# Optimization experiments

Measured on AMD Instinct MI355X. Metric: run time of the kernel, lower is better.

Reference implementation:

```python
import jax, jax.numpy as jnp
import numpy as np

N_NODES = 8192
IN_DIM = 512
H_DIM = 128


def setup_inputs() -> dict:
    key = jax.random.key(0)
    k1, k2, k3, k4 = jax.random.split(key, 4)
    h = jax.random.normal(k1, (N_NODES, IN_DIM), dtype=jnp.float32)
    adj = jax.random.randint(k2, (N_NODES, N_NODES), 0, 2).astype(jnp.float32)
    # xavier-uniform-style scales
    w_scale = float(np.sqrt(6.0 / (IN_DIM + H_DIM)))
    W_w = jax.random.uniform(k3, (H_DIM, IN_DIM), minval=-w_scale, maxval=w_scale, dtype=jnp.float32)
    W_b = jnp.zeros((H_DIM,), dtype=jnp.float32)
    a_scale = float(np.sqrt(6.0 / (1 + H_DIM)))
    a = jax.random.uniform(k4, (1, H_DIM), minval=-a_scale, maxval=a_scale, dtype=jnp.float32)
    return {"h": h, "adj": adj, "W_w": W_w, "W_b": W_b, "a": a}


def reference(h, adj, W_w, W_b, a):
    # Wh: (n, H)
    Wh = h @ W_w.T + W_b
    # (Wh_i + Wh_j) @ a.T == s_i + s_j with s = Wh @ a.T  -> avoids (n,n,H) intermediate
    s = Wh @ a[0]                                  # (n,)
    e = jax.nn.leaky_relu(s[:, None] + s[None, :], negative_slope=0.2)  # (n, n)
    mask = adj != 0
    e = jnp.where(mask, e, -jnp.inf)
    # safe row softmax; rows with no neighbors -> alpha row of zeros (matches nan_to_num)
    m = jnp.max(e, axis=1, keepdims=True)
    m_safe = jnp.where(jnp.isfinite(m), m, 0.0)
    ex = jnp.where(mask, jnp.exp(e - m_safe), 0.0)
    denom = jnp.sum(ex, axis=1, keepdims=True)
    alpha = ex / jnp.where(denom == 0, 1.0, denom)
    z = jax.nn.sigmoid(alpha @ Wh)                 # (n, H)
    return z, alpha
```

## Files before the change

kernel.cpp:

```cpp
#include <hip/hip_runtime.h>
#include <hip/hip_bf16.h>
#include <math.h>

#define N_NODES 8192
#define IN_DIM  512
#define H_DIM   128
#define KC      1024
#define NKB     (N_NODES / KC)
#define BMRA    128
#define NTW     (N_NODES / 64)
#define NB_WH   (N_NODES / 32)
#define NB_MASK (N_NODES / 4)
#define NB_A    ((N_NODES / BMRA) * NKB)
#define NB_B    (N_NODES / 4)

typedef __attribute__((ext_vector_type(8))) short bf16x8;
typedef __attribute__((ext_vector_type(4))) float f32x4;

__device__ __forceinline__ float lrelu(float x) { return fmaxf(x, 0.2f * x); }

__device__ __forceinline__ unsigned int f2mono(float x) {
    unsigned int b = __float_as_uint(x);
    return (b & 0x80000000u) ? ~b : (b | 0x80000000u);
}
__device__ __forceinline__ float mono2f(unsigned int u) {
    unsigned int b = (u & 0x80000000u) ? (u ^ 0x80000000u) : ~u;
    return __uint_as_float(b);
}

__device__ __forceinline__ short f2bf(float x) {
    union { __hip_bfloat16 h; short s; } cv;
    cv.h = __float2bfloat16(x);
    return cv.s;
}

__global__ __launch_bounds__(256) void k_wa(const float* __restrict__ Ww,
                                            const float* __restrict__ Wb,
                                            const float* __restrict__ a,
                                            float* __restrict__ wa,
                                            float* __restrict__ ba,
                                            unsigned int* __restrict__ smax) {
    const int t = threadIdx.x;
    #pragma unroll
    for (int kk = 0; kk < 2; ++kk) {
        int k = t + kk * 256;
        float sum = 0.f;
        #pragma unroll 8
        for (int c = 0; c < H_DIM; ++c)
            sum += Ww[(size_t)c * IN_DIM + k] * a[c];
        wa[k] = sum;
    }
    __shared__ float red[256];
    red[t] = (t < H_DIM) ? Wb[t] * a[t] : 0.f;
    __syncthreads();
    for (int off = 128; off > 0; off >>= 1) {
        if (t < off) red[t] += red[t + off];
        __syncthreads();
    }
    if (t == 0) { ba[0] = red[0]; *smax = 0u; }
}

__global__ __launch_bounds__(256) void k_s0(const float* __restrict__ h,
                                            const float* __restrict__ wa,
                                            const float* __restrict__ ba,
                                            float* __restrict__ s,
                                            unsigned int* __restrict__ smax) {
    const int w = threadIdx.x >> 6, lane = threadIdx.x & 63;
    const int row = blockIdx.x * 4 + w;
    const float* hp = h + (size_t)row * IN_DIM + lane * 8;
    f32x4 h0 = *(const f32x4*)(hp);
    f32x4 h1 = *(const f32x4*)(hp + 4);
    f32x4 w0 = *(const f32x4*)(wa + lane * 8);
    f32x4 w1 = *(const f32x4*)(wa + lane * 8 + 4);
    float v = h0[0]*w0[0] + h0[1]*w0[1] + h0[2]*w0[2] + h0[3]*w0[3]
            + h1[0]*w1[0] + h1[1]*w1[1] + h1[2]*w1[2] + h1[3]*w1[3];
    #pragma unroll
    for (int off = 32; off > 0; off >>= 1) v += __shfl_down(v, off);
    __shared__ float bmax[4];
    if (lane == 0) { float sv = v + ba[0]; s[row] = sv; bmax[w] = sv; }
    __syncthreads();
    if (threadIdx.x == 0) {
        float m = fmaxf(fmaxf(bmax[0], bmax[1]), fmaxf(bmax[2], bmax[3]));
        atomicMax(smax, f2mono(m));
    }
}

__global__ __launch_bounds__(256) void k_front2(const float* __restrict__ h,
                                                const float* __restrict__ Ww,
                                                const float* __restrict__ Wb,
                                                __hip_bfloat16* __restrict__ WhT2,
                                                const float* __restrict__ adj,
                                                unsigned long long* __restrict__ bm,
                                                const float* __restrict__ s,
                                                const unsigned int* __restrict__ smaxp,
                                                float* __restrict__ denom) {
    __shared__ float hT[64][32 + 4];
    __shared__ float wT[64][H_DIM + 4];
    const int tid = threadIdx.x;
    const int bx = blockIdx.x;

    if (bx < NB_WH) {
        const int w = tid >> 6, lane = tid & 63;
        const int trm = tid >> 5, tcm = tid & 31;
        const int row0 = bx * 32;

        float acc[4][4] = {};
        for (int k0 = 0; k0 < IN_DIM; k0 += 64) {
            __syncthreads();
            #pragma unroll
            for (int p = 0; p < 8; ++p) {
                int r = 4 * p + w;
                hT[lane][r] = h[(size_t)(row0 + r) * IN_DIM + k0 + lane];
            }
            #pragma unroll
            for (int p = 0; p < 32; ++p) {
                int c = 4 * p + w;
                wT[lane][c] = Ww[(size_t)c * IN_DIM + k0 + lane];
            }
            __syncthreads();
            #pragma unroll 8
            for (int kk = 0; kk < 64; ++kk) {
                f32x4 a4 = *(const f32x4*)&hT[kk][4 * trm];
                f32x4 b4 = *(const f32x4*)&wT[kk][4 * tcm];
                #pragma unroll
                for (int i = 0; i < 4; ++i)
                    #pragma unroll
                    for (int j = 0; j < 4; ++j)
                        acc[i][j] = fmaf(a4[i], b4[j], acc[i][j]);
            }
        }
        f32x4 wb4 = *(const f32x4*)&Wb[4 * tcm];
        #pragma unroll
        for (int i = 0; i < 4; ++i) {
            int row = row0 + 4 * trm + i;
            int ts = row >> 5, kq = (row >> 3) & 3, e = row & 7;
            #pragma unroll
            for (int jj = 0; jj < 4; ++jj) {
                int c = 4 * tcm + jj;
                int f = c >> 4, r16 = c & 15;
                WhT2[((size_t)(ts * 8 + f) * 64 + kq * 16 + r16) * 8 + e] =
                    __float2bfloat16(acc[i][jj] + wb4[jj]);
            }
        }
    } else {
        const int lane = tid & 63;
        const int row = (bx - NB_WH) * 4 + (tid >> 6);
        const float* arow = adj + (size_t)row * N_NODES;
        unsigned long long* mrow = bm + (size_t)row * NTW;
        const float smax = mono2f(*smaxp);
        const float si = s[row];
        const float mi = lrelu(si + smax);
        float dsum = 0.f;
        #pragma unroll 4
        for (int c = 0; c < N_NODES / 256; ++c) {
            int col = c * 256 + lane * 4;
            f32x4 a4 = __builtin_nontemporal_load((const f32x4*)(arow + col));
            f32x4 sj = *(const f32x4*)&s[col];
            unsigned long long v = 0ull;
            #pragma unroll
            for (int q = 0; q < 4; ++q) {
                bool nb = (a4[q] != 0.f);
                v |= nb ? (1ull << q) : 0ull;
                dsum += nb ? __expf(lrelu(si + sj[q]) - mi) : 0.f;
            }
            v <<= (4 * (lane & 15));
            v |= __shfl_xor(v, 1);
            v |= __shfl_xor(v, 2);
            v |= __shfl_xor(v, 4);
            v |= __shfl_xor(v, 8);
            if ((lane & 15) == 0)
                mrow[c * 4 + (lane >> 4)] = v;
        }
        #pragma unroll
        for (int off = 32; off > 0; off >>= 1) dsum += __shfl_down(dsum, off);
        if (lane == 0) denom[row] = dsum;
    }
}

__global__ __launch_bounds__(256) void k_mid(const unsigned long long* __restrict__ bm,
                                             const __hip_bfloat16* __restrict__ WhT2,
                                             const float* __restrict__ s,
                                             const unsigned int* __restrict__ smaxp,
                                             const float* __restrict__ denom,
                                             float* __restrict__ ypart,
                                             float* __restrict__ alpha) {
    const int tid = threadIdx.x;
    const int bx = blockIdx.x;
    const float smax = mono2f(*smaxp);

    if (bx < NB_A) {
        const int lane = tid & 63;
        const int w    = tid >> 6;
        const int r16  = lane & 15;
        const int kq   = lane >> 4;
        const int xb   = bx & 63;
        const int yb   = bx >> 6;
        const int rowB = xb * BMRA + w * 32;
        const int j0   = yb * KC;
        const int rowA0 = rowB + r16;
        const int rowA1 = rowB + 16 + r16;

        const float si0 = s[rowA0], si1 = s[rowA1];
        const float mi0 = lrelu(si0 + smax), mi1 = lrelu(si1 + smax);

        f32x4 acc0[8], acc1[8];
        {
            f32x4 zv = {0.f, 0.f, 0.f, 0.f};
            #pragma unroll
            for (int f = 0; f < 8; ++f) { acc0[f] = zv; acc1[f] = zv; }
        }
        const float* sp = s + j0 + kq * 8;
        const unsigned long long* mrow0 = bm + (size_t)rowA0 * NTW + (j0 >> 6);
        const unsigned long long* mrow1 = bm + (size_t)rowA1 * NTW + (j0 >> 6);

        for (int bs = 0; bs < KC / 64; ++bs) {
            unsigned long long m64a = mrow0[bs];
            unsigned long long m64b = mrow1[bs];
            #pragma unroll
            for (int sub = 0; sub < 2; ++sub) {
                const int ts = bs * 2 + sub;
                unsigned int bits0 = (unsigned int)(m64a >> (sub * 32 + kq * 8)) & 0xffu;
                unsigned int bits1 = (unsigned int)(m64b >> (sub * 32 + kq * 8)) & 0xffu;

                f32x4 sc0 = *(const f32x4*)(sp + ts * 32);
                f32x4 sc1 = *(const f32x4*)(sp + ts * 32 + 4);
                float sv[8] = {sc0[0], sc0[1], sc0[2], sc0[3], sc1[0], sc1[1], sc1[2], sc1[3]};
                bf16x8 af0, af1;
                #pragma unroll
                for (int e = 0; e < 8; ++e) {
                    float ex0 = ((bits0 >> e) & 1u) ? __expf(lrelu(si0 + sv[e]) - mi0) : 0.f;
                    float ex1 = ((bits1 >> e) & 1u) ? __expf(lrelu(si1 + sv[e]) - mi1) : 0.f;
                    af0[e] = f2bf(ex0);
                    af1[e] = f2bf(ex1);
                }
                const __hip_bfloat16* base =
                    WhT2 + (size_t)((j0 >> 5) + ts) * 4096 + lane * 8;
                #pragma unroll
                for (int half = 0; half < 2; ++half) {
                    bf16x8 bc[4];
                    #pragma unroll
                    for (int f = 0; f < 4; ++f)
                        bc[f] = *(const bf16x8*)(base + (half * 4 + f) * 512);
                    #pragma unroll
                    for (int f = 0; f < 4; ++f) {
                        acc0[half * 4 + f] =
                            __builtin_amdgcn_mfma_f32_16x16x32_bf16(af0, bc[f], acc0[half * 4 + f], 0, 0, 0);
                        acc1[half * 4 + f] =
                            __builtin_amdgcn_mfma_f32_16x16x32_bf16(af1, bc[f], acc1[half * 4 + f], 0, 0, 0);
                    }
                }
            }
        }
        float* yp = ypart + (size_t)yb * N_NODES * H_DIM;
        #pragma unroll
        for (int f = 0; f < 8; ++f)
            #pragma unroll
            for (int i = 0; i < 4; ++i) {
                int cc = f * 16 + r16;
                yp[(size_t)(rowB + kq * 4 + i) * H_DIM + cc] = acc0[f][i];
                yp[(size_t)(rowB + 16 + kq * 4 + i) * H_DIM + cc] = acc1[f][i];
            }
    } else {
        const int NSTEP = N_NODES / 256;
        const int w = tid >> 6, lane = tid & 63;
        const int row = (bx - NB_A) * 4 + w;
        const float si = s[row];
        const float mi = lrelu(si + smax);
        const float d = denom[row];
        const float rd = d > 0.f ? 1.f / d : 0.f;
        float* arow = alpha + (size_t)row * N_NODES;
        const unsigned long long* mrow = bm + (size_t)row * NTW;
        #pragma unroll 4
        for (int t = 0; t < NSTEP; ++t) {
            int col = t * 256 + lane * 4;
            unsigned long long mb = mrow[t * 4 + (lane >> 4)];
            int sh = (lane & 15) * 4;
            f32x4 sj = *(const f32x4*)&s[col];
            f32x4 o;
            o[0] = ((mb >> (sh + 0)) & 1ull) ? __expf(lrelu(si + sj[0]) - mi) * rd : 0.f;
            o[1] = ((mb >> (sh + 1)) & 1ull) ? __expf(lrelu(si + sj[1]) - mi) * rd : 0.f;
            o[2] = ((mb >> (sh + 2)) & 1ull) ? __expf(lrelu(si + sj[2]) - mi) * rd : 0.f;
            o[3] = ((mb >> (sh + 3)) & 1ull) ? __expf(lrelu(si + sj[3]) - mi) * rd : 0.f;
            __builtin_nontemporal_store(o, (f32x4*)&arow[col]);
        }
    }
}

__global__ __launch_bounds__(256) void k_z2(const float* __restrict__ ypart,
                                            const float* __restrict__ denom,
                                            float* __restrict__ z) {
    int i = blockIdx.x * 256 + threadIdx.x;
    int row = i >> 7;
    float d = denom[row];
    float rd = d > 0.f ? 1.f / d : 0.f;
    float v = 0.f;
    #pragma unroll
    for (int p = 0; p < NKB; ++p)
        v += ypart[(size_t)p * N_NODES * H_DIM + i];
    v *= rd;
    z[i] = 1.f / (1.f + __expf(-v));
}

__global__ __launch_bounds__(256) void k_zero(f32x4* __restrict__ p, int n16) {
    int i = blockIdx.x * 256 + threadIdx.x;
    if (i < n16) {
        f32x4 zv = {0.f, 0.f, 0.f, 0.f};
        __builtin_nontemporal_store(zv, p + i);
    }
}

__global__ __launch_bounds__(256) void k_wh_fb(const float* __restrict__ h,
                                               const float* __restrict__ Ww,
                                               const float* __restrict__ Wb,
                                               __hip_bfloat16* __restrict__ WhT2) {
    __shared__ float hT[64][32 + 4];
    __shared__ float wT[64][H_DIM + 4];
    const int tid = threadIdx.x;
    const int w = tid >> 6, lane = tid & 63;
    const int trm = tid >> 5, tcm = tid & 31;
    const int row0 = blockIdx.x * 32;

    float acc[4][4] = {};
    for (int k0 = 0; k0 < IN_DIM; k0 += 64) {
        __syncthreads();
        #pragma unroll
        for (int p = 0; p < 8; ++p) {
            int r = 4 * p + w;
            hT[lane][r] = h[(size_t)(row0 + r) * IN_DIM + k0 + lane];
        }
        #pragma unroll
        for (int p = 0; p < 32; ++p) {
            int c = 4 * p + w;
            wT[lane][c] = Ww[(size_t)c * IN_DIM + k0 + lane];
        }
        __syncthreads();
        #pragma unroll 8
        for (int kk = 0; kk < 64; ++kk) {
            f32x4 a4 = *(const f32x4*)&hT[kk][4 * trm];
            f32x4 b4 = *(const f32x4*)&wT[kk][4 * tcm];
            #pragma unroll
            for (int i = 0; i < 4; ++i)
                #pragma unroll
                for (int j = 0; j < 4; ++j)
                    acc[i][j] = fmaf(a4[i], b4[j], acc[i][j]);
        }
    }
    f32x4 wb4 = *(const f32x4*)&Wb[4 * tcm];
    #pragma unroll
    for (int i = 0; i < 4; ++i) {
        int row = row0 + 4 * trm + i;
        int ts = row >> 5, kq = (row >> 3) & 3, e = row & 7;
        #pragma unroll
        for (int jj = 0; jj < 4; ++jj) {
            int c = 4 * tcm + jj;
            int f = c >> 4, r16 = c & 15;
            WhT2[((size_t)(ts * 8 + f) * 64 + kq * 16 + r16) * 8 + e] =
                __float2bfloat16(acc[i][jj] + wb4[jj]);
        }
    }
}

__global__ __launch_bounds__(256) void k_A_fb(const float* __restrict__ adj,
                                              const __hip_bfloat16* __restrict__ WhT2,
                                              const float* __restrict__ s,
                                              const unsigned int* __restrict__ smaxp,
                                              float* __restrict__ denom,
                                              float* __restrict__ y) {
    __shared__ unsigned char msk[64 * 64];
    const int tid  = threadIdx.x;
    const int lane = tid & 63;
    const int w    = tid >> 6;
    const int r16  = lane & 15;
    const int kq   = lane >> 4;
    const int row0 = blockIdx.x * 64;
    const int j0base = blockIdx.y * KC;
    const int rowA = row0 + w * 16 + r16;

    const float smax = mono2f(*smaxp);
    const float si = s[rowA];
    const float mi = lrelu(si + smax);

    f32x4 acc[8];
    {
        f32x4 zv = {0.f, 0.f, 0.f, 0.f};
        #pragma unroll
        for (int f = 0; f < 8; ++f) acc[f] = zv;
    }
    float dsum = 0.f;
    const float* sp = s + j0base + kq * 8;

    int sRow[4], sCol[4];
    #pragma unroll
    for (int p = 0; p < 4; ++p) {
        int seg = p * 256 + tid;
        sRow[p] = seg >> 4;
        sCol[p] = (seg & 15) * 4;
    }
    const int NBIG = KC / 64;
    f32x4 areg[4];
    #pragma unroll
    for (int p = 0; p < 4; ++p)
        areg[p] = __builtin_nontemporal_load(
            (const f32x4*)(adj + (size_t)(row0 + sRow[p]) * N_NODES + j0base + sCol[p]));

    for (int bs = 0; bs < NBIG; ++bs) {
        __syncthreads();
        #pragma unroll
        for (int p = 0; p < 4; ++p) {
            f32x4 a4 = areg[p];
            unsigned int mwd = 0u;
            mwd |= (a4[0] != 0.f) ? 0x00000001u : 0u;
            mwd |= (a4[1] != 0.f) ? 0x00000100u : 0u;
            mwd |= (a4[2] != 0.f) ? 0x00010000u : 0u;
            mwd |= (a4[3] != 0.f) ? 0x01000000u : 0u;
            int r = sRow[p], c = sCol[p];
            int slot = (c >> 3) ^ (r & 7);
            *(unsigned int*)&msk[r * 64 + (slot << 3) + (c & 7)] = mwd;
        }
        __syncthreads();
        if (bs + 1 < NBIG) {
            const int j1 = j0base + (bs + 1) * 64;
            #pragma unroll
            for (int p = 0; p < 4; ++p)
                areg[p] = __builtin_nontemporal_load(
                    (const f32x4*)(adj + (size_t)(row0 + sRow[p]) * N_NODES + j1 + sCol[p]));
        }
        #pragma unroll
        for (int sub = 0; sub < 2; ++sub) {
            const int ts = bs * 2 + sub;
            const int rT = w * 16 + r16;
            const int slotR = (sub * 4 + kq) ^ (r16 & 7);
            unsigned long long m8 = *(const unsigned long long*)&msk[rT * 64 + (slotR << 3)];
            unsigned int bits = (unsigned int)((m8 * 0x0102040810204080ull) >> 56) & 0xffu;

            f32x4 sc0 = *(const f32x4*)(sp + ts * 32);
            f32x4 sc1 = *(const f32x4*)(sp + ts * 32 + 4);
            float sv[8] = {sc0[0], sc0[1], sc0[2], sc0[3], sc1[0], sc1[1], sc1[2], sc1[3]};
            bf16x8 afrag;
            #pragma unroll
            for (int e = 0; e < 8; ++e) {
                bool nb = (bits >> e) & 1u;
                float ex = nb ? __expf(lrelu(si + sv[e]) - mi) : 0.f;
                dsum += ex;
                afrag[e] = f2bf(ex);
            }
            const __hip_bfloat16* base =
                WhT2 + (size_t)((j0base >> 5) + ts) * 4096 + lane * 8;
            #pragma unroll
            for (int half = 0; half < 2; ++half) {
                bf16x8 bc[4];
                #pragma unroll
                for (int f = 0; f < 4; ++f)
                    bc[f] = *(const bf16x8*)(base + (half * 4 + f) * 512);
                #pragma unroll
                for (int f = 0; f < 4; ++f)
                    acc[half * 4 + f] =
                        __builtin_amdgcn_mfma_f32_16x16x32_bf16(afrag, bc[f], acc[half * 4 + f], 0, 0, 0);
            }
        }
    }
    {
        float v = dsum;
        v += __shfl_xor(v, 16);
        v += __shfl_xor(v, 32);
        if (lane < 16) atomicAdd(&denom[row0 + w * 16 + lane], v);
    }
    #pragma unroll
    for (int f = 0; f < 8; ++f)
        #pragma unroll
        for (int i = 0; i < 4; ++i) {
            int rr = row0 + w * 16 + kq * 4 + i;
            int cc = f * 16 + r16;
            atomicAdd(&y[(size_t)rr * H_DIM + cc], acc[f][i]);
        }
}

__global__ __launch_bounds__(256) void k_B_fb(const float* __restrict__ adj,
                                              const float* __restrict__ s,
                                              const float* __restrict__ denom,
                                              const unsigned int* __restrict__ smaxp,
                                              float* __restrict__ alpha) {
    const int NSTEP = N_NODES / 256;
    const int w = threadIdx.x >> 6, lane = threadIdx.x & 63;
    const int row = blockIdx.x * 4 + w;
    const float smax = mono2f(*smaxp);
    const float si = s[row];
    const float mi = lrelu(si + smax);
    const float d = denom[row];
    const float rd = d > 0.f ? 1.f / d : 0.f;
    float* arow = alpha + (size_t)row * N_NODES;
    const float* adjrow = adj + (size_t)row * N_NODES;
    #pragma unroll 4
    for (int t = 0; t < NSTEP; ++t) {
        int col = t * 256 + lane * 4;
        f32x4 a4 = __builtin_nontemporal_load((const f32x4*)&adjrow[col]);
        f32x4 sj = *(const f32x4*)&s[col];
        f32x4 o;
        o[0] = (a4[0] != 0.f) ? __expf(lrelu(si + sj[0]) - mi) * rd : 0.f;
        o[1] = (a4[1] != 0.f) ? __expf(lrelu(si + sj[1]) - mi) * rd : 0.f;
        o[2] = (a4[2] != 0.f) ? __expf(lrelu(si + sj[2]) - mi) * rd : 0.f;
        o[3] = (a4[3] != 0.f) ? __expf(lrelu(si + sj[3]) - mi) * rd : 0.f;
        __builtin_nontemporal_store(o, (f32x4*)&arow[col]);
    }
}

__global__ __launch_bounds__(256) void k_z_fb(const float* __restrict__ y,
                                              const float* __restrict__ denom,
                                              float* __restrict__ z) {
    int i = blockIdx.x * 256 + threadIdx.x;
    int row = i >> 7;
    float d = denom[row];
    float rd = d > 0.f ? 1.f / d : 0.f;
    float v = y[i] * rd;
    z[i] = 1.f / (1.f + __expf(-v));
}

extern "C" void kernel_launch(void* const* d_in, const int* in_sizes, int n_in,
                              void* d_out, int out_size, void* d_ws, size_t ws_size,
                              hipStream_t stream) {
    const float* h   = (const float*)d_in[0];
    const float* adj = (const float*)d_in[1];
    const float* Ww  = (const float*)d_in[2];
    const float* Wb  = (const float*)d_in[3];
    const float* a   = (const float*)d_in[4];

    float* z     = (float*)d_out;
    float* alpha = z + (size_t)N_NODES * H_DIM;

    char* ws = (char*)d_ws;
    float* y     = (float*)ws;  ws += sizeof(float) * (size_t)N_NODES * H_DIM;
    float* denom = (float*)ws;  ws += sizeof(float) * N_NODES;
    unsigned int* smax = (unsigned int*)ws;  ws += 256;
    size_t zero_bytes = (size_t)(ws - (char*)d_ws);
    float* wa    = (float*)ws;  ws += sizeof(float) * IN_DIM;
    float* ba    = (float*)ws;  ws += 256;
    __hip_bfloat16* WhT2 = (__hip_bfloat16*)ws;
    ws += sizeof(__hip_bfloat16) * (size_t)N_NODES * H_DIM;
    float* s     = (float*)ws;  ws += sizeof(float) * N_NODES;
    unsigned long long* bmask = (unsigned long long*)ws;
    ws += (size_t)N_NODES * NTW * sizeof(unsigned long long);
    float* ypart = (float*)ws;
    ws += (size_t)NKB * N_NODES * H_DIM * sizeof(float);
    size_t full_need = (size_t)(ws - (char*)d_ws);
    int use_full = (ws_size >= full_need) ? 1 : 0;

    hipLaunchKernelGGL(k_wa, dim3(1), dim3(256), 0, stream, Ww, Wb, a, wa, ba, smax);
    hipLaunchKernelGGL(k_s0, dim3(N_NODES / 4), dim3(256), 0, stream, h, wa, ba, s, smax);

    if (use_full) {
        hipLaunchKernelGGL(k_front2, dim3(NB_WH + NB_MASK), dim3(256), 0, stream,
                           h, Ww, Wb, WhT2, adj, bmask, s, smax, denom);
        hipLaunchKernelGGL(k_mid, dim3(NB_A + NB_B), dim3(256), 0, stream,
                           bmask, WhT2, s, smax, denom, ypart, alpha);
        hipLaunchKernelGGL(k_z2, dim3((N_NODES * H_DIM) / 256), dim3(256), 0, stream,
                           ypart, denom, z);
    } else {
        int n16 = (int)(zero_bytes / 16);
        hipLaunchKernelGGL(k_zero, dim3((n16 + 255) / 256), dim3(256), 0, stream,
                           (f32x4*)d_ws, n16);
        hipLaunchKernelGGL(k_wh_fb, dim3(NB_WH), dim3(256), 0, stream, h, Ww, Wb, WhT2);
        hipLaunchKernelGGL(k_A_fb, dim3(N_NODES / 64, NKB), dim3(256), 0, stream,
                           adj, WhT2, s, smax, denom, y);
        hipLaunchKernelGGL(k_B_fb, dim3(N_NODES / 4), dim3(256), 0, stream,
                           adj, s, denom, smax, alpha);
        hipLaunchKernelGGL(k_z_fb, dim3((N_NODES * H_DIM) / 256), dim3(256), 0, stream,
                           y, denom, z);
    }
}
```

Measured before the change: 231.7 us.

## Halve per-wave rows in aggregation and interleave matmul with alpha-write blocks

Each wave in the aggregation part of k_mid now handles 16 rows instead of 32, which doubles the number of matmul blocks and reduces accumulator register pressure. Block indices are interleaved so that every third block does the masked-exp MFMA aggregation and the other two write alpha rows. The aim is to mix compute-bound and store-bound blocks on each CU at the same time, rather than running all matmul blocks before all store blocks. In exchange, each loaded WhT tile is reused for half as many rows, so global/L2 traffic for WhT doubles.

```diff
diff --git a/kernel.cpp b/kernel.cpp
--- a/kernel.cpp
+++ b/kernel.cpp
@@ -7,11 +7,10 @@
 #define H_DIM   128
 #define KC      1024
 #define NKB     (N_NODES / KC)
-#define BMRA    128
 #define NTW     (N_NODES / 64)
 #define NB_WH   (N_NODES / 32)
 #define NB_MASK (N_NODES / 4)
-#define NB_A    ((N_NODES / BMRA) * NKB)
+#define NB_A    ((N_NODES / 64) * NKB)
 #define NB_B    (N_NODES / 4)
 
 typedef __attribute__((ext_vector_type(8))) short bf16x8;
@@ -187,51 +186,47 @@
     const int tid = threadIdx.x;
     const int bx = blockIdx.x;
     const float smax = mono2f(*smaxp);
-
-    if (bx < NB_A) {
+    const int mod = bx % 3;
+
+    if (mod == 0) {
+        const int aid  = bx / 3;
+        const int xb   = aid & 127;
+        const int yb   = aid >> 7;
         const int lane = tid & 63;
         const int w    = tid >> 6;
         const int r16  = lane & 15;
         const int kq   = lane >> 4;
-        const int xb   = bx & 63;
-        const int yb   = bx >> 6;
-        const int rowB = xb * BMRA + w * 32;
+        const int rowB = xb * 64 + w * 16;
         const int j0   = yb * KC;
-        const int rowA0 = rowB + r16;
-        const int rowA1 = rowB + 16 + r16;
-
-        const float si0 = s[rowA0], si1 = s[rowA1];
-        const float mi0 = lrelu(si0 + smax), mi1 = lrelu(si1 + smax);
-
-        f32x4 acc0[8], acc1[8];
+        const int rowA = rowB + r16;
+
+        const float si = s[rowA];
+        const float mi = lrelu(si + smax);
+
+        f32x4 acc[8];
         {
             f32x4 zv = {0.f, 0.f, 0.f, 0.f};
             #pragma unroll
-            for (int f = 0; f < 8; ++f) { acc0[f] = zv; acc1[f] = zv; }
+            for (int f = 0; f < 8; ++f) acc[f] = zv;
         }
         const float* sp = s + j0 + kq * 8;
-        const unsigned long long* mrow0 = bm + (size_t)rowA0 * NTW + (j0 >> 6);
-        const unsigned long long* mrow1 = bm + (size_t)rowA1 * NTW + (j0 >> 6);
+        const unsigned long long* mrow = bm + (size_t)rowA * NTW + (j0 >> 6);
 
         for (int bs = 0; bs < KC / 64; ++bs) {
-            unsigned long long m64a = mrow0[bs];
-            unsigned long long m64b = mrow1[bs];
+            unsigned long long m64 = mrow[bs];
             #pragma unroll
             for (int sub = 0; sub < 2; ++sub) {
                 const int ts = bs * 2 + sub;
-                unsigned int bits0 = (unsigned int)(m64a >> (sub * 32 + kq * 8)) & 0xffu;
-                unsigned int bits1 = (unsigned int)(m64b >> (sub * 32 + kq * 8)) & 0xffu;
+                unsigned int bits = (unsigned int)(m64 >> (sub * 32 + kq * 8)) & 0xffu;
 
                 f32x4 sc0 = *(const f32x4*)(sp + ts * 32);
                 f32x4 sc1 = *(const f32x4*)(sp + ts * 32 + 4);
                 float sv[8] = {sc0[0], sc0[1], sc0[2], sc0[3], sc1[0], sc1[1], sc1[2], sc1[3]};
-                bf16x8 af0, af1;
+                bf16x8 af;
                 #pragma unroll
                 for (int e = 0; e < 8; ++e) {
-                    float ex0 = ((bits0 >> e) & 1u) ? __expf(lrelu(si0 + sv[e]) - mi0) : 0.f;
-                    float ex1 = ((bits1 >> e) & 1u) ? __expf(lrelu(si1 + sv[e]) - mi1) : 0.f;
-                    af0[e] = f2bf(ex0);
-                    af1[e] = f2bf(ex1);
+                    float ex = ((bits >> e) & 1u) ? __expf(lrelu(si + sv[e]) - mi) : 0.f;
+                    af[e] = f2bf(ex);
                 }
                 const __hip_bfloat16* base =
                     WhT2 + (size_t)((j0 >> 5) + ts) * 4096 + lane * 8;
@@ -242,12 +237,9 @@
                     for (int f = 0; f < 4; ++f)
                         bc[f] = *(const bf16x8*)(base + (half * 4 + f) * 512);
                     #pragma unroll
-                    for (int f = 0; f < 4; ++f) {
-                        acc0[half * 4 + f] =
-                            __builtin_amdgcn_mfma_f32_16x16x32_bf16(af0, bc[f], acc0[half * 4 + f], 0, 0, 0);
-                        acc1[half * 4 + f] =
-                            __builtin_amdgcn_mfma_f32_16x16x32_bf16(af1, bc[f], acc1[half * 4 + f], 0, 0, 0);
-                    }
+                    for (int f = 0; f < 4; ++f)
+                        acc[half * 4 + f] =
+                            __builtin_amdgcn_mfma_f32_16x16x32_bf16(af, bc[f], acc[half * 4 + f], 0, 0, 0);
                 }
             }
         }
@@ -257,13 +249,13 @@
             #pragma unroll
             for (int i = 0; i < 4; ++i) {
                 int cc = f * 16 + r16;
-                yp[(size_t)(rowB + kq * 4 + i) * H_DIM + cc] = acc0[f][i];
-                yp[(size_t)(rowB + 16 + kq * 4 + i) * H_DIM + cc] = acc1[f][i];
+                yp[(size_t)(rowB + kq * 4 + i) * H_DIM + cc] = acc[f][i];
             }
     } else {
+        const int bid = (bx / 3) * 2 + (mod - 1);
         const int NSTEP = N_NODES / 256;
         const int w = tid >> 6, lane = tid & 63;
-        const int row = (bx - NB_A) * 4 + w;
+        const int row = bid * 4 + w;
         const float si = s[row];
         const float mi = lrelu(si + smax);
         const float d = denom[row];
```

New measurement: 242.7 us. +4.8%, slower.

## Fuse alpha row write into mask/denominator pass, keep mask bits in registers

Applied to the files above, without the earlier changes.

The alpha-writing row pass moves out of the middle kernel into the front kernel. Each wave keeps its row's adjacency bits in registers (mybits) and writes the normalized alpha right after reducing the denominator, using an xor all-reduce so every lane holds the sum. This avoids re-reading the bitmask and denominator, and the middle kernel now runs only the MFMA aggregation. The cost is that the front kernel grows heavier and does more serial work per row, and the overlap between the alpha stores and the MFMA blocks is lost.

```diff
diff --git a/kernel.cpp b/kernel.cpp
--- a/kernel.cpp
+++ b/kernel.cpp
@@ -7,12 +7,10 @@
 #define H_DIM   128
 #define KC      1024
 #define NKB     (N_NODES / KC)
-#define BMRA    128
 #define NTW     (N_NODES / 64)
 #define NB_WH   (N_NODES / 32)
-#define NB_MASK (N_NODES / 4)
-#define NB_A    ((N_NODES / BMRA) * NKB)
-#define NB_B    (N_NODES / 4)
+#define NB_ROW  (N_NODES / 4)
+#define NB_A2   ((N_NODES / 128) * NKB)
 
 typedef __attribute__((ext_vector_type(8))) short bf16x8;
 typedef __attribute__((ext_vector_type(4))) float f32x4;
@@ -85,15 +83,16 @@
     }
 }
 
-__global__ __launch_bounds__(256) void k_front2(const float* __restrict__ h,
-                                                const float* __restrict__ Ww,
-                                                const float* __restrict__ Wb,
-                                                __hip_bfloat16* __restrict__ WhT2,
-                                                const float* __restrict__ adj,
-                                                unsigned long long* __restrict__ bm,
-                                                const float* __restrict__ s,
-                                                const unsigned int* __restrict__ smaxp,
-                                                float* __restrict__ denom) {
+__global__ __launch_bounds__(256) void k_rowfront(const float* __restrict__ h,
+                                                  const float* __restrict__ Ww,
+                                                  const float* __restrict__ Wb,
+                                                  __hip_bfloat16* __restrict__ WhT2,
+                                                  const float* __restrict__ adj,
+                                                  unsigned long long* __restrict__ bm,
+                                                  const float* __restrict__ s,
+                                                  const unsigned int* __restrict__ smaxp,
+                                                  float* __restrict__ denom,
+                                                  float* __restrict__ alpha) {
     __shared__ float hT[64][32 + 4];
     __shared__ float wT[64][H_DIM + 4];
     const int tid = threadIdx.x;
@@ -151,19 +150,22 @@
         const float si = s[row];
         const float mi = lrelu(si + smax);
         float dsum = 0.f;
+        unsigned int mybits[4] = {0u, 0u, 0u, 0u};
+
         #pragma unroll 4
         for (int c = 0; c < N_NODES / 256; ++c) {
             int col = c * 256 + lane * 4;
             f32x4 a4 = __builtin_nontemporal_load((const f32x4*)(arow + col));
             f32x4 sj = *(const f32x4*)&s[col];
-            unsigned long long v = 0ull;
+            unsigned int b4 = 0u;
             #pragma unroll
             for (int q = 0; q < 4; ++q) {
                 bool nb = (a4[q] != 0.f);
-                v |= nb ? (1ull << q) : 0ull;
+                b4 |= nb ? (1u << q) : 0u;
                 dsum += nb ? __expf(lrelu(si + sj[q]) - mi) : 0.f;
             }
-            v <<= (4 * (lane & 15));
+            mybits[c >> 3] |= b4 << ((c & 7) * 4);
+            unsigned long long v = (unsigned long long)b4 << (4 * (lane & 15));
             v |= __shfl_xor(v, 1);
             v |= __shfl_xor(v, 2);
             v |= __shfl_xor(v, 4);
@@ -172,118 +174,103 @@
                 mrow[c * 4 + (lane >> 4)] = v;
         }
         #pragma unroll
-        for (int off = 32; off > 0; off >>= 1) dsum += __shfl_down(dsum, off);
+        for (int off = 1; off < 64; off <<= 1) dsum += __shfl_xor(dsum, off);
         if (lane == 0) denom[row] = dsum;
-    }
-}
-
-__global__ __launch_bounds__(256) void k_mid(const unsigned long long* __restrict__ bm,
-                                             const __hip_bfloat16* __restrict__ WhT2,
-                                             const float* __restrict__ s,
-                                             const unsigned int* __restrict__ smaxp,
-                                             const float* __restrict__ denom,
-                                             float* __restrict__ ypart,
-                                             float* __restrict__ alpha) {
-    const int tid = threadIdx.x;
-    const int bx = blockIdx.x;
-    const float smax = mono2f(*smaxp);
-
-    if (bx < NB_A) {
-        const int lane = tid & 63;
-        const int w    = tid >> 6;
-        const int r16  = lane & 15;
-        const int kq   = lane >> 4;
-        const int xb   = bx & 63;
-        const int yb   = bx >> 6;
-        const int rowB = xb * BMRA + w * 32;
-        const int j0   = yb * KC;
-        const int rowA0 = rowB + r16;
-        const int rowA1 = rowB + 16 + r16;
-
-        const float si0 = s[rowA0], si1 = s[rowA1];
-        const float mi0 = lrelu(si0 + smax), mi1 = lrelu(si1 + smax);
-
-        f32x4 acc0[8], acc1[8];
-        {
-            f32x4 zv = {0.f, 0.f, 0.f, 0.f};
-            #pragma unroll
-            for (int f = 0; f < 8; ++f) { acc0[f] = zv; acc1[f] = zv; }
-        }
-        const float* sp = s + j0 + kq * 8;
-        const unsigned long long* mrow0 = bm + (size_t)rowA0 * NTW + (j0 >> 6);
-        const unsigned long long* mrow1 = bm + (size_t)rowA1 * NTW + (j0 >> 6);
-
-        for (int bs = 0; bs < KC / 64; ++bs) {
-            unsigned long long m64a = mrow0[bs];
-            unsigned long long m64b = mrow1[bs];
-            #pragma unroll
-            for (int sub = 0; sub < 2; ++sub) {
-                const int ts = bs * 2 + sub;
-                unsigned int bits0 = (unsigned int)(m64a >> (sub * 32 + kq * 8)) & 0xffu;
-                unsigned int bits1 = (unsigned int)(m64b >> (sub * 32 + kq * 8)) & 0xffu;
-
-                f32x4 sc0 = *(const f32x4*)(sp + ts * 32);
-                f32x4 sc1 = *(const f32x4*)(sp + ts * 32 + 4);
-                float sv[8] = {sc0[0], sc0[1], sc0[2], sc0[3], sc1[0], sc1[1], sc1[2], sc1[3]};
-                bf16x8 af0, af1;
-                #pragma unroll
-                for (int e = 0; e < 8; ++e) {
-                    float ex0 = ((bits0 >> e) & 1u) ? __expf(lrelu(si0 + sv[e]) - mi0) : 0.f;
-                    float ex1 = ((bits1 >> e) & 1u) ? __expf(lrelu(si1 + sv[e]) - mi1) : 0.f;
-                    af0[e] = f2bf(ex0);
-                    af1[e] = f2bf(ex1);
-                }
-                const __hip_bfloat16* base =
-                    WhT2 + (size_t)((j0 >> 5) + ts) * 4096 + lane * 8;
-                #pragma unroll
-                for (int half = 0; half < 2; ++half) {
-                    bf16x8 bc[4];
-                    #pragma unroll
-                    for (int f = 0; f < 4; ++f)
-                        bc[f] = *(const bf16x8*)(base + (half * 4 + f) * 512);
-                    #pragma unroll
-                    for (int f = 0; f < 4; ++f) {
-                        acc0[half * 4 + f] =
-                            __builtin_amdgcn_mfma_f32_16x16x32_bf16(af0, bc[f], acc0[half * 4 + f], 0, 0, 0);
-                        acc1[half * 4 + f] =
-                            __builtin_amdgcn_mfma_f32_16x16x32_bf16(af1, bc[f], acc1[half * 4 + f], 0, 0, 0);
-                    }
-                }
-            }
-        }
-        float* yp = ypart + (size_t)yb * N_NODES * H_DIM;
-        #pragma unroll
-        for (int f = 0; f < 8; ++f)
-            #pragma unroll
-            for (int i = 0; i < 4; ++i) {
-                int cc = f * 16 + r16;
-                yp[(size_t)(rowB + kq * 4 + i) * H_DIM + cc] = acc0[f][i];
-                yp[(size_t)(rowB + 16 + kq * 4 + i) * H_DIM + cc] = acc1[f][i];
-            }
-    } else {
-        const int NSTEP = N_NODES / 256;
-        const int w = tid >> 6, lane = tid & 63;
-        const int row = (bx - NB_A) * 4 + w;
-        const float si = s[row];
-        const float mi = lrelu(si + smax);
-        const float d = denom[row];
-        const float rd = d > 0.f ? 1.f / d : 0.f;
-        float* arow = alpha + (size_t)row * N_NODES;
-        const unsigned long long* mrow = bm + (size_t)row * NTW;
+        const float rd = dsum > 0.f ? 1.f / dsum : 0.f;
+
+        float* arw = alpha + (size_t)row * N_NODES;
         #pragma unroll 4
-        for (int t = 0; t < NSTEP; ++t) {
-            int col = t * 256 + lane * 4;
-            unsigned long long mb = mrow[t * 4 + (lane >> 4)];
-            int sh = (lane & 15) * 4;
+        for (int c = 0; c < N_NODES / 256; ++c) {
+            int col = c * 256 + lane * 4;
+            unsigned int b4 = (mybits[c >> 3] >> ((c & 7) * 4)) & 0xfu;
             f32x4 sj = *(const f32x4*)&s[col];
             f32x4 o;
-            o[0] = ((mb >> (sh + 0)) & 1ull) ? __expf(lrelu(si + sj[0]) - mi) * rd : 0.f;
-            o[1] = ((mb >> (sh + 1)) & 1ull) ? __expf(lrelu(si + sj[1]) - mi) * rd : 0.f;
-            o[2] = ((mb >> (sh + 2)) & 1ull) ? __expf(lrelu(si + sj[2]) - mi) * rd : 0.f;
-            o[3] = ((mb >> (sh + 3)) & 1ull) ? __expf(lrelu(si + sj[3]) - mi) * rd : 0.f;
-            __builtin_nontemporal_store(o, (f32x4*)&arow[col]);
-        }
-    }
+            o[0] = (b4 & 1u) ? __expf(lrelu(si + sj[0]) - mi) * rd : 0.f;
+            o[1] = (b4 & 2u) ? __expf(lrelu(si + sj[1]) - mi) * rd : 0.f;
+            o[2] = (b4 & 4u) ? __expf(lrelu(si + sj[2]) - mi) * rd : 0.f;
+            o[3] = (b4 & 8u) ? __expf(lrelu(si + sj[3]) - mi) * rd : 0.f;
+            __builtin_nontemporal_store(o, (f32x4*)&arw[col]);
+        }
+    }
+}
+
+__global__ __launch_bounds__(256) void k_A(const unsigned long long* __restrict__ bm,
+                                           const __hip_bfloat16* __restrict__ WhT2,
+                                           const float* __restrict__ s,
+                                           const unsigned int* __restrict__ smaxp,
+                                           float* __restrict__ ypart) {
+    const int lane = threadIdx.x & 63;
+    const int w    = threadIdx.x >> 6;
+    const int r16  = lane & 15;
+    const int kq   = lane >> 4;
+    const int xb   = blockIdx.x & 63;
+    const int yb   = blockIdx.x >> 6;
+    const int rowB = xb * 128 + w * 32;
+    const int j0   = yb * KC;
+    const int rowA0 = rowB + r16;
+    const int rowA1 = rowB + 16 + r16;
+
+    const float smax = mono2f(*smaxp);
+    const float si0 = s[rowA0], si1 = s[rowA1];
+    const float mi0 = lrelu(si0 + smax), mi1 = lrelu(si1 + smax);
+
+    f32x4 acc0[8], acc1[8];
+    {
+        f32x4 zv = {0.f, 0.f, 0.f, 0.f};
+        #pragma unroll
+        for (int f = 0; f < 8; ++f) { acc0[f] = zv; acc1[f] = zv; }
+    }
+    const float* sp = s + j0 + kq * 8;
+    const unsigned long long* mrow0 = bm + (size_t)rowA0 * NTW + (j0 >> 6);
+    const unsigned long long* mrow1 = bm + (size_t)rowA1 * NTW + (j0 >> 6);
+
+    for (int bs = 0; bs < KC / 64; ++bs) {
+        unsigned long long m64a = mrow0[bs];
+        unsigned long long m64b = mrow1[bs];
+        #pragma unroll
+        for (int sub = 0; sub < 2; ++sub) {
+            const int ts = bs * 2 + sub;
+            unsigned int bits0 = (unsigned int)(m64a >> (sub * 32 + kq * 8)) & 0xffu;
+            unsigned int bits1 = (unsigned int)(m64b >> (sub * 32 + kq * 8)) & 0xffu;
+
+            f32x4 sc0 = *(const f32x4*)(sp + ts * 32);
+            f32x4 sc1 = *(const f32x4*)(sp + ts * 32 + 4);
+            float sv[8] = {sc0[0], sc0[1], sc0[2], sc0[3], sc1[0], sc1[1], sc1[2], sc1[3]};
+            bf16x8 af0, af1;
+            #pragma unroll
+            for (int e = 0; e < 8; ++e) {
+                float ex0 = ((bits0 >> e) & 1u) ? __expf(lrelu(si0 + sv[e]) - mi0) : 0.f;
+                float ex1 = ((bits1 >> e) & 1u) ? __expf(lrelu(si1 + sv[e]) - mi1) : 0.f;
+                af0[e] = f2bf(ex0);
+                af1[e] = f2bf(ex1);
+            }
+            const __hip_bfloat16* base =
+                WhT2 + (size_t)((j0 >> 5) + ts) * 4096 + lane * 8;
+            #pragma unroll
+            for (int half = 0; half < 2; ++half) {
+                bf16x8 bc[4];
+                #pragma unroll
+                for (int f = 0; f < 4; ++f)
+                    bc[f] = *(const bf16x8*)(base + (half * 4 + f) * 512);
+                #pragma unroll
+                for (int f = 0; f < 4; ++f) {
+                    acc0[half * 4 + f] =
+                        __builtin_amdgcn_mfma_f32_16x16x32_bf16(af0, bc[f], acc0[half * 4 + f], 0, 0, 0);
+                    acc1[half * 4 + f] =
+                        __builtin_amdgcn_mfma_f32_16x16x32_bf16(af1, bc[f], acc1[half * 4 + f], 0, 0, 0);
+                }
+            }
+        }
+    }
+    float* yp = ypart + (size_t)yb * N_NODES * H_DIM;
+    #pragma unroll
+    for (int f = 0; f < 8; ++f)
+        #pragma unroll
+        for (int i = 0; i < 4; ++i) {
+            int cc = f * 16 + r16;
+            yp[(size_t)(rowB + kq * 4 + i) * H_DIM + cc] = acc0[f][i];
+            yp[(size_t)(rowB + 16 + kq * 4 + i) * H_DIM + cc] = acc1[f][i];
+        }
 }
 
 __global__ __launch_bounds__(256) void k_z2(const float* __restrict__ ypart,
@@ -548,10 +535,10 @@
     hipLaunchKernelGGL(k_s0, dim3(N_NODES / 4), dim3(256), 0, stream, h, wa, ba, s, smax);
 
     if (use_full) {
-        hipLaunchKernelGGL(k_front2, dim3(NB_WH + NB_MASK), dim3(256), 0, stream,
-                           h, Ww, Wb, WhT2, adj, bmask, s, smax, denom);
-        hipLaunchKernelGGL(k_mid, dim3(NB_A + NB_B), dim3(256), 0, stream,
-                           bmask, WhT2, s, smax, denom, ypart, alpha);
+        hipLaunchKernelGGL(k_rowfront, dim3(NB_WH + NB_ROW), dim3(256), 0, stream,
+                           h, Ww, Wb, WhT2, adj, bmask, s, smax, denom, alpha);
+        hipLaunchKernelGGL(k_A, dim3(NB_A2), dim3(256), 0, stream,
+                           bmask, WhT2, s, smax, ypart);
         hipLaunchKernelGGL(k_z2, dim3((N_NODES * H_DIM) / 256), dim3(256), 0, stream,
                            ypart, denom, z);
     } else {
```

Measured after the change: 266.3 us. 14.9% more time.
